# Optimization experiments

Measured on AMD Instinct MI355X. Metric: run time of the kernel, lower is better.

Reference implementation:

```python
import jax, jax.numpy as jnp
import numpy as np

NCE_T = 0.07


def setup_inputs() -> dict:
    key = jax.random.key(0)
    k1, k2, k3 = jax.random.split(key, 3)
    features_1 = jax.random.normal(k1, (1, 20000, 256), dtype=jnp.float32)
    features_2 = jax.random.normal(k2, (1, 8192, 256), dtype=jnp.float32)
    map21 = jax.random.randint(k3, (8192,), 0, 20000, dtype=jnp.int64)
    return {"features_1": features_1, "features_2": features_2, "map21": map21}


def reference(features_1, features_2, map21):
    # squeeze leading batch dim (module assumes batch size 1)
    f1 = features_1[0]  # [N1, D]
    f2 = features_2[0]  # [P, D]  (P == nce_num_pairs == len(map21) -> arange branch)
    query = f1[map21]   # [P, D] gather
    keys = f2           # [P, D]
    # pairwise Euclidean distance via matmul trick (matches torch.cdist p=2)
    q_sq = jnp.sum(query * query, axis=-1)  # [P]
    k_sq = jnp.sum(keys * keys, axis=-1)    # [P]
    sq_dist = q_sq[:, None] + k_sq[None, :] - 2.0 * (query @ keys.T)  # [P, P]
    dist = jnp.sqrt(jnp.maximum(sq_dist, 0.0))
    logits = -dist / NCE_T
    # cross entropy with labels = arange(P): mean of -log_softmax diagonal
    logp = jax.nn.log_softmax(logits, axis=-1)
    loss = -jnp.mean(jnp.diagonal(logp))
    return loss
```

## Files before the change

### kernel.cpp

```cpp
#include <hip/hip_runtime.h>
#include <hip/hip_bf16.h>

#define PP      8192
#define DIM     256
#define DIMP    272
#define NKF     17
#define GS      (32 * DIMP)
#define NCHUNK  16
#define TCOLS   16
#define ROWBLK  128
#define NROWBLK (PP / ROWBLK)
#define TILEB   (32 * DIMP * 2)
#define NBUF    2

typedef __bf16 bf16_t;
using bf16x8 = __attribute__((ext_vector_type(8))) __bf16;
using bf16x4 = __attribute__((ext_vector_type(4))) __bf16;
using f32x4  = __attribute__((ext_vector_type(4))) float;
using f32x16 = __attribute__((ext_vector_type(16))) float;

typedef __attribute__((address_space(1))) void as1_void;
typedef __attribute__((address_space(3))) void as3_void;

#define C2    20.609929155556618
#define MEXP  (-340.0f)
#define COEF  ((float)(-(C2 * 1.4142135623730951) * 8388608.0))
#define KBIAS ((float)((127.0 + 340.0) * 8388608.0))
#define LN2   0.6931471805599453f

__global__ __launch_bounds__(256) void nce_prep(
    const float* __restrict__ f1, const float* __restrict__ f2,
    const int* __restrict__ map,
    bf16_t* __restrict__ qb2, bf16_t* __restrict__ kb2,
    float* __restrict__ diag2, float* __restrict__ part_l,
    unsigned* __restrict__ cnt, float* __restrict__ out)
{
    const int tid  = threadIdx.x;
    const int wave = tid >> 6, lane = tid & 63;
    const int p    = blockIdx.x * 4 + wave;
    const int gtid = blockIdx.x * 256 + tid;

    if (gtid < PP) part_l[gtid] = 0.0f;
    if (gtid < NROWBLK) cnt[gtid] = 0u;
    if (gtid == 0) out[0] = 0.0f;

    const int idx = map[p];
    const f32x4 qv = *(const f32x4*)(f1 + (size_t)idx * DIM + lane * 4);
    const f32x4 kv = *(const f32x4*)(f2 + (size_t)p * DIM + lane * 4);

    float qs = qv[0]*qv[0] + qv[1]*qv[1] + qv[2]*qv[2] + qv[3]*qv[3];
    float ks = kv[0]*kv[0] + kv[1]*kv[1] + kv[2]*kv[2] + kv[3]*kv[3];
    const f32x4 dv = qv - kv;
    float ds = dv[0]*dv[0] + dv[1]*dv[1] + dv[2]*dv[2] + dv[3]*dv[3];

    bf16x4 qo, ko;
    #pragma unroll
    for (int i = 0; i < 4; ++i) { qo[i] = (bf16_t)qv[i]; ko[i] = (bf16_t)kv[i]; }

    const int G = p >> 5, l31 = p & 31;
    const int kk = lane >> 2, h = (lane >> 1) & 1, j0 = (lane & 1) * 4;
    const size_t base = (size_t)G * GS;
    const size_t off  = base + (size_t)(kk * 64 + h * 32 + l31) * 8 + j0;
    *(bf16x4*)(qb2 + off) = qo;
    *(bf16x4*)(kb2 + off) = ko;

    #pragma unroll
    for (int s = 32; s > 0; s >>= 1) {
        qs += __shfl_xor(qs, s);
        ks += __shfl_xor(ks, s);
        ds += __shfl_xor(ds, s);
    }

    if (lane < 4) {
        const int hh = lane & 1;
        bf16x8 v;
        #pragma unroll
        for (int i = 0; i < 8; ++i) v[i] = (bf16_t)0.0f;
        if (lane == 0) {
            const float qh = -0.5f * qs;
            const bf16_t q1 = (bf16_t)qh;
            v[0] = q1; v[1] = (bf16_t)(qh - (float)q1);
            v[2] = (bf16_t)1.0f; v[3] = (bf16_t)1.0f;
        } else if (lane == 2) {
            const float kh = -0.5f * ks;
            const bf16_t k1 = (bf16_t)kh;
            v[0] = (bf16_t)1.0f; v[1] = (bf16_t)1.0f;
            v[2] = k1; v[3] = (bf16_t)(kh - (float)k1);
        }
        bf16_t* dstp = (lane < 2) ? qb2 : kb2;
        *(bf16x8*)(dstp + base + (size_t)(1024 + hh * 32 + l31) * 8) = v;
    }
    if (lane == 0)
        diag2[p] = (float)(-C2) * __builtin_amdgcn_sqrtf(ds);
}

__device__ __forceinline__ void stage(const bf16_t* __restrict__ kb2,
                                      int Gc, int wave, int lane, char* dst)
{
    __builtin_assume(wave >= 0 && wave < 4);
    __builtin_assume(lane >= 0 && lane < 64);
    const bf16_t* src = kb2 + (size_t)Gc * GS + wave * 512 + lane * 8;
    char* d = dst + wave * 1024;
    #pragma unroll
    for (int j = 0; j < 4; ++j)
        __builtin_amdgcn_global_load_lds((const as1_void*)(src + j * 2048),
                                         (as3_void*)(d + j * 4096), 16, 0, 0);
    if (wave == 0)
        __builtin_amdgcn_global_load_lds((const as1_void*)(src + 4 * 2048),
                                         (as3_void*)(d + 4 * 4096), 16, 0, 0);
}

#define PHASE(NW, DOPRE, T)                                                    \
  do {                                                                         \
    asm volatile("s_waitcnt lgkmcnt(0)\n\ts_barrier" ::: "memory");            \
    if (DOPRE) stage(kb2, c0g + (T) + 1, wave, lane, smem[((T) + 1) & 1]);     \
    asm volatile("s_waitcnt vmcnt(%c0)" :: "i"(NW) : "memory");                \
    const bf16_t* bp = (const bf16_t*)smem[(T) & 1] + lane * 8;                \
    f32x16 acc = {0,0,0,0,0,0,0,0,0,0,0,0,0,0,0,0};                           \
    __builtin_amdgcn_s_setprio(1);                                             \
    _Pragma("unroll")                                                          \
    for (int kk = 0; kk < NKF; ++kk) {                                         \
        const bf16x8 b = *(const bf16x8*)(bp + kk * 512);                      \
        acc = __builtin_amdgcn_mfma_f32_32x32x16_bf16(a[kk], b, acc, 0, 0, 0); \
    }                                                                          \
    __builtin_amdgcn_s_setprio(0);                                             \
         \
    _Pragma("unroll")                                                          \
    for (int i = 0; i < 16; ++i) {                                             \
        const float tt = __builtin_amdgcn_sqrtf(-acc[i]);                      \
        const float uu = fmaxf(fmaf(tt, COEF, KBIAS), 0.0f);                   \
        l[i] += __uint_as_float((unsigned)uu);                                 \
    }                                                                          \
  } while (0)

__global__ __launch_bounds__(256, 4) void nce_main(
    const bf16_t* __restrict__ qb2, const bf16_t* __restrict__ kb2,
    const float* __restrict__ diag2, float* __restrict__ part_l,
    unsigned* __restrict__ cnt, float* __restrict__ out)
{
    const int tid  = threadIdx.x, wave = tid >> 6, lane = tid & 63;
    const int l31  = lane & 31, h = lane >> 5;

    const int lin = blockIdx.x + (blockIdx.y << 6);
    const int xcd = lin & 7, idx = lin >> 3;
    const int rb  = (xcd & 3) * 16 + (idx & 15);
    const int cy  = (xcd >> 2) * 8 + (idx >> 4);
    const int G0  = rb * 4 + wave;
    const int c0g = cy * TCOLS;

    __shared__ __align__(16) char smem[NBUF][TILEB];
    __shared__ int s_last;
    __shared__ float red[4];

    stage(kb2, c0g, wave, lane, smem[0]);

    bf16x8 a[NKF];
    {
        const bf16_t* ap = qb2 + (size_t)G0 * GS + lane * 8;
        #pragma unroll
        for (int kk = 0; kk < NKF; ++kk)
            a[kk] = *(const bf16x8*)(ap + kk * 512);
    }

    float l[16];
    #pragma unroll
    for (int i = 0; i < 16; ++i) l[i] = 0.0f;

    #pragma unroll 1
    for (int t = 0; t < TCOLS - 1; ++t)
        PHASE(4, true, t);
    PHASE(0, false, TCOLS - 1);

    #pragma unroll
    for (int s = 1; s < 32; s <<= 1) {
        #pragma unroll
        for (int i = 0; i < 16; ++i)
            l[i] += __shfl_xor(l[i], s);
    }

    if (l31 == 0) {
        #pragma unroll
        for (int i = 0; i < 16; ++i) {
            const int r = (i & 3) + 8 * (i >> 2) + 4 * h;
            atomicAdd(&part_l[G0 * 32 + r], l[i]);
        }
    }

    __syncthreads();
    if (tid == 0) {
        __threadfence();
        s_last = (atomicAdd(&cnt[rb], 1u) == NCHUNK - 1) ? 1 : 0;
    }
    __syncthreads();
    if (s_last) {
        float v = 0.0f;
        if (tid < ROWBLK) {
            const int row = rb * ROWBLK + tid;
            const float lf = atomicAdd(&part_l[row], 0.0f);
            v = MEXP + __builtin_amdgcn_logf(lf) - diag2[row];
        }
        #pragma unroll
        for (int s = 1; s < 64; s <<= 1) v += __shfl_xor(v, s);
        if (lane == 0) red[wave] = v;
        __syncthreads();
        if (tid == 0)
            atomicAdd(out, (red[0] + red[1] + red[2] + red[3]) * (LN2 / (float)PP));
    }
}

extern "C" void kernel_launch(void* const* d_in, const int* in_sizes, int n_in,
                              void* d_out, int out_size, void* d_ws, size_t ws_size,
                              hipStream_t stream)
{
    const float* f1  = (const float*)d_in[0];
    const float* f2  = (const float*)d_in[1];
    const int*   map = (const int*)d_in[2];
    float* out = (float*)d_out;

    char* ws = (char*)d_ws;
    bf16_t*   qb2    = (bf16_t*)ws;
    bf16_t*   kb2    = qb2 + (size_t)256 * GS;
    float*    diag2  = (float*)(ws + 2ull * 256 * GS * sizeof(bf16_t));
    float*    part_l = diag2 + PP;
    unsigned* cnt    = (unsigned*)(part_l + PP);

    nce_prep<<<PP / 4, 256, 0, stream>>>(f1, f2, map, qb2, kb2, diag2,
                                         part_l, cnt, out);
    nce_main<<<dim3(NROWBLK, NCHUNK), 256, 0, stream>>>(qb2, kb2, diag2,
                                                        part_l, cnt, out);
}
```

Before: 128.0 us.

## Process two column tiles per phase with halved column-chunk grid

After: 122.0 us. 4.7% less time.

```diff
diff --git a/kernel.cpp b/kernel.cpp
--- a/kernel.cpp
+++ b/kernel.cpp
@@ -6,8 +6,8 @@
 #define DIMP    272
 #define NKF     17
 #define GS      (32 * DIMP)
-#define NCHUNK  16
-#define TCOLS   16
+#define NCHUNK  8
+#define PHASES  16
 #define ROWBLK  128
 #define NROWBLK (PP / ROWBLK)
 #define TILEB   (32 * DIMP * 2)
@@ -110,30 +110,37 @@
                                          (as3_void*)(d + 4 * 4096), 16, 0, 0);
 }
 
-#define PHASE(NW, DOPRE, T)                                                    \
+#define PHASE(DOPRE, T)                                                        \
   do {                                                                         \
-    asm volatile("s_waitcnt lgkmcnt(0)\n\ts_barrier" ::: "memory");            \
-    if (DOPRE) stage(kb2, c0g + (T) + 1, wave, lane, smem[((T) + 1) & 1]);     \
-    asm volatile("s_waitcnt vmcnt(%c0)" :: "i"(NW) : "memory");                \
-    const bf16_t* bp = (const bf16_t*)smem[(T) & 1] + lane * 8;                \
-    f32x16 acc = {0,0,0,0,0,0,0,0,0,0,0,0,0,0,0,0};                           \
-    __builtin_amdgcn_s_setprio(1);                                             \
+    if (DOPRE) {                                                               \
+        stage(kb2, c0g + 2 * ((T) + 1),     wave, lane, smem[((T)+1) & 1][0]); \
+        stage(kb2, c0g + 2 * ((T) + 1) + 1, wave, lane, smem[((T)+1) & 1][1]); \
+    }                                                                          \
+    const bf16_t* bp0 = (const bf16_t*)smem[(T) & 1][0] + lane * 8;            \
+    const bf16_t* bp1 = (const bf16_t*)smem[(T) & 1][1] + lane * 8;            \
+    f32x16 acc0 = {0,0,0,0,0,0,0,0,0,0,0,0,0,0,0,0};                          \
+    f32x16 acc1 = {0,0,0,0,0,0,0,0,0,0,0,0,0,0,0,0};                          \
     _Pragma("unroll")                                                          \
     for (int kk = 0; kk < NKF; ++kk) {                                         \
-        const bf16x8 b = *(const bf16x8*)(bp + kk * 512);                      \
-        acc = __builtin_amdgcn_mfma_f32_32x32x16_bf16(a[kk], b, acc, 0, 0, 0); \
+        const bf16x8 b0 = *(const bf16x8*)(bp0 + kk * 512);                    \
+        const bf16x8 b1 = *(const bf16x8*)(bp1 + kk * 512);                    \
+        acc0 = __builtin_amdgcn_mfma_f32_32x32x16_bf16(a[kk], b0, acc0,0,0,0); \
+        acc1 = __builtin_amdgcn_mfma_f32_32x32x16_bf16(a[kk], b1, acc1,0,0,0); \
     }                                                                          \
-    __builtin_amdgcn_s_setprio(0);                                             \
-         \
+      \
+      \
     _Pragma("unroll")                                                          \
     for (int i = 0; i < 16; ++i) {                                             \
-        const float tt = __builtin_amdgcn_sqrtf(-acc[i]);                      \
-        const float uu = fmaxf(fmaf(tt, COEF, KBIAS), 0.0f);                   \
-        l[i] += __uint_as_float((unsigned)uu);                                 \
+        const float t0 = __builtin_amdgcn_sqrtf(-acc0[i]);                     \
+        const float u0 = fmaxf(fmaf(t0, COEF, KBIAS), 0.0f);                   \
+        const float t1 = __builtin_amdgcn_sqrtf(-acc1[i]);                     \
+        const float u1 = fmaxf(fmaf(t1, COEF, KBIAS), 0.0f);                   \
+        l[i] += __uint_as_float((unsigned)u0) + __uint_as_float((unsigned)u1); \
     }                                                                          \
+    asm volatile("s_waitcnt vmcnt(0) lgkmcnt(0)\n\ts_barrier" ::: "memory");   \
   } while (0)
 
-__global__ __launch_bounds__(256, 4) void nce_main(
+__global__ __launch_bounds__(256, 2) void nce_main(
     const bf16_t* __restrict__ qb2, const bf16_t* __restrict__ kb2,
     const float* __restrict__ diag2, float* __restrict__ part_l,
     unsigned* __restrict__ cnt, float* __restrict__ out)
@@ -144,15 +151,16 @@
     const int lin = blockIdx.x + (blockIdx.y << 6);
     const int xcd = lin & 7, idx = lin >> 3;
     const int rb  = (xcd & 3) * 16 + (idx & 15);
-    const int cy  = (xcd >> 2) * 8 + (idx >> 4);
+    const int cy  = (xcd >> 2) * 4 + (idx >> 4);
     const int G0  = rb * 4 + wave;
-    const int c0g = cy * TCOLS;
-
-    __shared__ __align__(16) char smem[NBUF][TILEB];
+    const int c0g = cy * (2 * PHASES);
+
+    __shared__ __align__(16) char smem[NBUF][2][TILEB];
     __shared__ int s_last;
     __shared__ float red[4];
 
-    stage(kb2, c0g, wave, lane, smem[0]);
+    stage(kb2, c0g,     wave, lane, smem[0][0]);
+    stage(kb2, c0g + 1, wave, lane, smem[0][1]);
 
     bf16x8 a[NKF];
     {
@@ -166,10 +174,12 @@
     #pragma unroll
     for (int i = 0; i < 16; ++i) l[i] = 0.0f;
 
+    asm volatile("s_waitcnt vmcnt(0) lgkmcnt(0)\n\ts_barrier" ::: "memory");
+
     #pragma unroll 1
-    for (int t = 0; t < TCOLS - 1; ++t)
-        PHASE(4, true, t);
-    PHASE(0, false, TCOLS - 1);
+    for (int t = 0; t < PHASES - 1; ++t)
+        PHASE(true, t);
+    PHASE(false, PHASES - 1);
 
     #pragma unroll
     for (int s = 1; s < 32; s <<= 1) {
```
